# Kernel tuning notes

Measured on AMD Instinct MI355X. Metric: run time of the kernel, lower is better.

The kernel has to match this reference:

```python
import jax, jax.numpy as jnp
import numpy as np

B = 4096
INPUT_DIM = 4096
N_BLOCKS = 8
BLOCK = INPUT_DIM // N_BLOCKS  # 512
N_EXPERTS = 6
H = 1024   # expert_hidden
H2 = H // 2


def setup_inputs() -> dict:
    key = jax.random.key(0)
    ks = jax.random.split(key, 16)
    s = 0.02  # init scale keeps tanh/softmax in sane range
    return {
        "x":   jax.random.normal(ks[0], (B, INPUT_DIM), jnp.float32),
        # routers: per-block stacked weights [8, ...]
        "Wr1": jax.random.normal(ks[1], (N_BLOCKS, BLOCK, 32), jnp.float32) * s,
        "br1": jax.random.normal(ks[2], (N_BLOCKS, 32), jnp.float32) * s,
        "Wr2": jax.random.normal(ks[3], (N_BLOCKS, 32, N_EXPERTS), jnp.float32) * s,
        "br2": jax.random.normal(ks[4], (N_BLOCKS, N_EXPERTS), jnp.float32) * s,
        # experts: stacked [6, ...], shared across all 8 blocks
        "We1": jax.random.normal(ks[5], (N_EXPERTS, BLOCK, H), jnp.float32) * s,
        "be1": jax.random.normal(ks[6], (N_EXPERTS, H), jnp.float32) * s,
        "We2": jax.random.normal(ks[7], (N_EXPERTS, H, H2), jnp.float32) * s,
        "be2": jax.random.normal(ks[8], (N_EXPERTS, H2), jnp.float32) * s,
        "We3": jax.random.normal(ks[9], (N_EXPERTS, H2, 3), jnp.float32) * s,
        "be3": jax.random.normal(ks[10], (N_EXPERTS, 3), jnp.float32) * s,
        # aggregator
        "Wa1": jax.random.normal(ks[11], (3, 16), jnp.float32) * s,
        "ba1": jax.random.normal(ks[12], (16,), jnp.float32) * s,
        "Wa2": jax.random.normal(ks[13], (16, 3), jnp.float32) * s,
        "ba2": jax.random.normal(ks[14], (3,), jnp.float32) * s,
    }


def reference(x, Wr1, br1, Wr2, br2, We1, be1, We2, be2, We3, be3,
              Wa1, ba1, Wa2, ba2):
    b = x.shape[0]
    blocks = x.reshape(b, N_BLOCKS, BLOCK)                       # [b,s,d]
    # routers (one per block s)
    r1 = jax.nn.relu(jnp.einsum('bsd,sdh->bsh', blocks, Wr1) + br1)
    routing = jax.nn.softmax(
        jnp.einsum('bsh,she->bse', r1, Wr2) + br2, axis=-1)      # [b,s,E]
    # experts applied to every block (grouped GEMMs)
    h1 = jnp.tanh(jnp.einsum('bsd,edh->bseh', blocks, We1) + be1)        # [b,s,E,H]
    h2 = jnp.tanh(jnp.einsum('bseh,ehk->bsek', h1, We2) + be2)           # [b,s,E,H2]
    eo = jnp.einsum('bsek,eko->bseo', h2, We3) + be3                     # [b,s,E,3]
    weighted = jnp.einsum('bse,bseo->bso', routing, eo)                  # [b,s,3]
    final = weighted.mean(axis=1)                                        # mean over 8 blocks
    a1 = jax.nn.relu(final @ Wa1 + ba1)
    return a1 @ Wa2 + ba2                                                # [b,3]
```

## Files before the change

kernel.cpp:

```cpp
#include <hip/hip_runtime.h>
#include <cstdint>
#include <cstddef>

typedef __bf16 bf16;
typedef __bf16 bf16x4 __attribute__((ext_vector_type(4)));
typedef __bf16 bf16x8 __attribute__((ext_vector_type(8)));
typedef float  f32x4  __attribute__((ext_vector_type(4)));

#define NROWS   32768
#define DBLK    512
#define H1N     1024
#define H2N     512
#define NEXP    6
#define NBATCH  4096
#define HALL    (NEXP * H1N)

__device__ __forceinline__ void gld16(const void* g, void* l) {
    __builtin_amdgcn_global_load_lds(
        (const __attribute__((address_space(1))) void*)g,
        (__attribute__((address_space(3))) void*)l, 16, 0, 0);
}

__device__ __forceinline__ float fast_tanh(float x) {
    float e = __expf(2.0f * x);
    return 1.0f - __fdividef(2.0f, e + 1.0f);
}

__device__ __forceinline__ float hsum16(float v) {
    v += __shfl_xor(v, 1);
    v += __shfl_xor(v, 2);
    v += __shfl_xor(v, 4);
    v += __shfl_xor(v, 8);
    return v;
}

__device__ __forceinline__ int swz(int row, int g) {
    return row * 64 + ((g ^ (row & 7)) * 8);
}


__global__ void cvt_bf16_kernel(const float* __restrict__ in,
                                bf16* __restrict__ out, int n4) {
    int i = blockIdx.x * blockDim.x + threadIdx.x;
    if (i >= n4) return;
    float4 v = ((const float4*)in)[i];
    bf16x4 o;
    o.x = (bf16)v.x; o.y = (bf16)v.y; o.z = (bf16)v.z; o.w = (bf16)v.w;
    ((bf16x4*)out)[i] = o;
}

__global__ __launch_bounds__(256) void transpose_cvt(
    const float* __restrict__ in, bf16* __restrict__ out, int K, int N) {
    __shared__ bf16 tile[64][66];
    int e  = blockIdx.z;
    int n0 = blockIdx.x * 64;
    int k0 = blockIdx.y * 64;
    int c  = threadIdx.x & 63;
    int rb = threadIdx.x >> 6;
    const float* src = in + (size_t)e * K * N;
    bf16* dst = out + (size_t)e * N * K;
#pragma unroll
    for (int it = 0; it < 16; ++it) {
        int k = k0 + rb + it * 4;
        int n = n0 + c;
        if (k < K && n < N) tile[rb + it * 4][c] = (bf16)src[(size_t)k * N + n];
    }
    __syncthreads();
#pragma unroll
    for (int it = 0; it < 16; ++it) {
        int n = n0 + rb + it * 4;
        int k = k0 + c;
        if (n < N && k < K) dst[(size_t)n * K + k] = tile[c][rb + it * 4];
    }
}

__global__ void zero_f32_kernel(float* __restrict__ p, int n) {
    int i = blockIdx.x * blockDim.x + threadIdx.x;
    if (i < n) p[i] = 0.0f;
}


__global__ __launch_bounds__(256, 2) void router_kernel(
    const bf16* __restrict__ xbf,
    const bf16* __restrict__ Wr1t,
    const float* __restrict__ br1,
    const float* __restrict__ Wr2,
    const float* __restrict__ br2,
    float* __restrict__ routing) {
    __shared__ __align__(16) bf16 sA[128 * 64];
    __shared__ __align__(16) bf16 sB[32 * 64];
    const int tid = threadIdx.x;
    const int w = tid >> 6, l = tid & 63;
    const int s  = blockIdx.y;
    const int b0 = blockIdx.x * 128;
    const int wm = w * 32;
    const int srow = l >> 3, schk = (l & 7) * 8;
    const int fr = l & 15, fq = l >> 4;
    const bf16* Ab = xbf + (size_t)s * 512;
    const bf16* Bb = Wr1t + (size_t)s * (32 * 512);

    f32x4 acc[2][2];
#pragma unroll
    for (int i = 0; i < 2; ++i)
#pragma unroll
        for (int j = 0; j < 2; ++j) acc[i][j] = (f32x4){0.f, 0.f, 0.f, 0.f};

    for (int k0 = 0; k0 < 512; k0 += 64) {
        __syncthreads();
#pragma unroll
        for (int jj = 0; jj < 4; ++jj) {
            int row = w * 32 + jj * 8;
            gld16(Ab + (size_t)(b0 + row + srow) * 4096 + k0 + schk, sA + row * 64);
        }
        gld16(Bb + (size_t)(w * 8 + srow) * 512 + k0 + schk, sB + w * 8 * 64);
        __syncthreads();
#pragma unroll
        for (int ks = 0; ks < 2; ++ks) {
            bf16x8 af[2], bfr[2];
#pragma unroll
            for (int i = 0; i < 2; ++i)
                af[i] = *(const bf16x8*)&sA[(wm + i * 16 + fr) * 64 + ks * 32 + fq * 8];
#pragma unroll
            for (int j = 0; j < 2; ++j)
                bfr[j] = *(const bf16x8*)&sB[(j * 16 + fr) * 64 + ks * 32 + fq * 8];
#pragma unroll
            for (int i = 0; i < 2; ++i)
#pragma unroll
                for (int j = 0; j < 2; ++j)
                    acc[i][j] = __builtin_amdgcn_mfma_f32_16x16x32_bf16(
                        af[i], bfr[j], acc[i][j], 0, 0, 0);
        }
    }

    float b1v[2], w2v[2][6], br2v[6];
#pragma unroll
    for (int j = 0; j < 2; ++j) {
        int col = j * 16 + fr;
        b1v[j] = br1[s * 32 + col];
#pragma unroll
        for (int e2 = 0; e2 < 6; ++e2) w2v[j][e2] = Wr2[(s * 32 + col) * 6 + e2];
    }
#pragma unroll
    for (int e2 = 0; e2 < 6; ++e2) br2v[e2] = br2[s * 6 + e2];

#pragma unroll
    for (int i = 0; i < 2; ++i) {
#pragma unroll
        for (int r = 0; r < 4; ++r) {
            float lg[6] = {0.f, 0.f, 0.f, 0.f, 0.f, 0.f};
#pragma unroll
            for (int j = 0; j < 2; ++j) {
                float t = fmaxf(acc[i][j][r] + b1v[j], 0.f);
#pragma unroll
                for (int e2 = 0; e2 < 6; ++e2) lg[e2] += t * w2v[j][e2];
            }
#pragma unroll
            for (int e2 = 0; e2 < 6; ++e2) lg[e2] = hsum16(lg[e2]) + br2v[e2];
            float mx = lg[0];
#pragma unroll
            for (int e2 = 1; e2 < 6; ++e2) mx = fmaxf(mx, lg[e2]);
            float p[6], sum = 0.f;
#pragma unroll
            for (int e2 = 0; e2 < 6; ++e2) { p[e2] = __expf(lg[e2] - mx); sum += p[e2]; }
            float inv = __fdividef(1.f, sum);
            if (fr == 0) {
                int brow = b0 + wm + i * 16 + fq * 4 + r;
                float* dst = routing + ((size_t)brow * 8 + s) * 6;
#pragma unroll
                for (int e2 = 0; e2 < 6; ++e2) dst[e2] = p[e2] * inv;
            }
        }
    }
}

__global__ __launch_bounds__(256, 4) void gemm1_kernel(
    const bf16* __restrict__ A,
    const bf16* __restrict__ B,
    const float* __restrict__ bias,
    bf16* __restrict__ h1,
    int chunk_rows) {
    __shared__ __align__(16) bf16 sA[128 * 64];
    __shared__ __align__(16) bf16 sB[128 * 64];
    const int tid = threadIdx.x;
    const int w = tid >> 6, l = tid & 63;
    const int n0 = blockIdx.x * 128;
    const int m0 = blockIdx.y * 128;
    const int wm = (w & 1) * 64, wn = (w >> 1) * 64;
    const int srow = l >> 3;
    const int gcol = ((l & 7) ^ srow) * 8;
    const int fr = l & 15, fq = l >> 4;
    const int eb = m0 >> 10;
    bf16* h1e = h1 + (size_t)eb * chunk_rows * H1N;
    const int mloc = m0 & 1023;

    f32x4 acc[4][4];
#pragma unroll
    for (int i = 0; i < 4; ++i)
#pragma unroll
        for (int j = 0; j < 4; ++j) acc[i][j] = (f32x4){0.f, 0.f, 0.f, 0.f};

    for (int k0 = 0; k0 < DBLK; k0 += 64) {
        __syncthreads();
#pragma unroll
        for (int jj = 0; jj < 4; ++jj) {
            int row = w * 32 + jj * 8;
            gld16(A + (size_t)(m0 + row + srow) * DBLK + k0 + gcol, sA + row * 64);
            gld16(B + (size_t)(n0 + row + srow) * DBLK + k0 + gcol, sB + row * 64);
        }
        __syncthreads();
#pragma unroll
        for (int ks = 0; ks < 2; ++ks) {
            bf16x8 af[4], bfr[4];
#pragma unroll
            for (int i = 0; i < 4; ++i)
                af[i] = *(const bf16x8*)&sA[swz(wm + i * 16 + fr, ks * 4 + fq)];
#pragma unroll
            for (int j = 0; j < 4; ++j)
                bfr[j] = *(const bf16x8*)&sB[swz(wn + j * 16 + fr, ks * 4 + fq)];
#pragma unroll
            for (int i = 0; i < 4; ++i)
#pragma unroll
                for (int j = 0; j < 4; ++j)
                    acc[i][j] = __builtin_amdgcn_mfma_f32_16x16x32_bf16(
                        af[i], bfr[j], acc[i][j], 0, 0, 0);
        }
    }

#pragma unroll
    for (int i = 0; i < 4; ++i) {
        int colb = m0 + wm + i * 16 + fq * 4;
        int cloc = mloc + wm + i * 16 + fq * 4;
        float4 bb = *(const float4*)&bias[colb];
#pragma unroll
        for (int j = 0; j < 4; ++j) {
            int xrow = n0 + wn + j * 16 + fr;
            bf16x4 o;
            o.x = (bf16)fast_tanh(acc[i][j][0] + bb.x);
            o.y = (bf16)fast_tanh(acc[i][j][1] + bb.y);
            o.z = (bf16)fast_tanh(acc[i][j][2] + bb.z);
            o.w = (bf16)fast_tanh(acc[i][j][3] + bb.w);
            *(bf16x4*)&h1e[(size_t)xrow * H1N + cloc] = o;
        }
    }
}

__global__ __launch_bounds__(256, 4) void gemm2_kernel(
    const bf16* __restrict__ h1,
    const bf16* __restrict__ W2t,
    const float* __restrict__ be2,
    const float* __restrict__ We3,
    float* __restrict__ eo,
    int chunk_rows, int row0) {
    __shared__ __align__(16) bf16 sA[128 * 64];
    __shared__ __align__(16) bf16 sB[128 * 64];
    __shared__ float w3s[128 * 3];
    __shared__ float b2s[128];
    const int tid = threadIdx.x;
    const int w = tid >> 6, l = tid & 63;
    const int e  = blockIdx.z;
    const int n0 = blockIdx.x * 128;
    const int m0 = blockIdx.y * 128;
    const int wm = (w & 1) * 64, wn = (w >> 1) * 64;
    const int srow = l >> 3;
    const int gcol = ((l & 7) ^ srow) * 8;
    const int fr = l & 15, fq = l >> 4;
    const bf16* Ae = W2t + (size_t)e * (H2N * H1N);
    const bf16* Be = h1 + (size_t)e * chunk_rows * H1N;

    if (tid < 128) {
        int c = m0 + tid;
        b2s[tid] = be2[e * H2N + c];
        w3s[tid * 3 + 0] = We3[((size_t)e * H2N + c) * 3 + 0];
        w3s[tid * 3 + 1] = We3[((size_t)e * H2N + c) * 3 + 1];
        w3s[tid * 3 + 2] = We3[((size_t)e * H2N + c) * 3 + 2];
    }

    f32x4 acc[4][4];
#pragma unroll
    for (int i = 0; i < 4; ++i)
#pragma unroll
        for (int j = 0; j < 4; ++j) acc[i][j] = (f32x4){0.f, 0.f, 0.f, 0.f};

    for (int k0 = 0; k0 < H1N; k0 += 64) {
        __syncthreads();
#pragma unroll
        for (int jj = 0; jj < 4; ++jj) {
            int row = w * 32 + jj * 8;
            gld16(Ae + (size_t)(m0 + row + srow) * H1N + k0 + gcol, sA + row * 64);
            gld16(Be + (size_t)(n0 + row + srow) * H1N + k0 + gcol, sB + row * 64);
        }
        __syncthreads();
#pragma unroll
        for (int ks = 0; ks < 2; ++ks) {
            bf16x8 af[4], bfr[4];
#pragma unroll
            for (int i = 0; i < 4; ++i)
                af[i] = *(const bf16x8*)&sA[swz(wm + i * 16 + fr, ks * 4 + fq)];
#pragma unroll
            for (int j = 0; j < 4; ++j)
                bfr[j] = *(const bf16x8*)&sB[swz(wn + j * 16 + fr, ks * 4 + fq)];
#pragma unroll
            for (int i = 0; i < 4; ++i)
#pragma unroll
                for (int j = 0; j < 4; ++j)
                    acc[i][j] = __builtin_amdgcn_mfma_f32_16x16x32_bf16(
                        af[i], bfr[j], acc[i][j], 0, 0, 0);
        }
    }

    float p[4][3];
#pragma unroll
    for (int j = 0; j < 4; ++j) { p[j][0] = 0.f; p[j][1] = 0.f; p[j][2] = 0.f; }
#pragma unroll
    for (int i = 0; i < 4; ++i) {
        int cl = wm + i * 16 + fq * 4;
        float4 bb = *(const float4*)&b2s[cl];
        float4 wa = *(const float4*)&w3s[cl * 3 + 0];
        float4 wb = *(const float4*)&w3s[cl * 3 + 4];
        float4 wc = *(const float4*)&w3s[cl * 3 + 8];
        float bias4[4] = {bb.x, bb.y, bb.z, bb.w};
        float w30[4] = {wa.x, wa.w, wb.z, wc.y};
        float w31[4] = {wa.y, wb.x, wb.w, wc.z};
        float w32[4] = {wa.z, wb.y, wc.x, wc.w};
#pragma unroll
        for (int j = 0; j < 4; ++j) {
#pragma unroll
            for (int r = 0; r < 4; ++r) {
                float t = fast_tanh(acc[i][j][r] + bias4[r]);
                p[j][0] += t * w30[r];
                p[j][1] += t * w31[r];
                p[j][2] += t * w32[r];
            }
        }
    }
#pragma unroll
    for (int j = 0; j < 4; ++j) {
        float v0 = p[j][0], v1 = p[j][1], v2 = p[j][2];
        v0 += __shfl_xor(v0, 16); v0 += __shfl_xor(v0, 32);
        v1 += __shfl_xor(v1, 16); v1 += __shfl_xor(v1, 32);
        v2 += __shfl_xor(v2, 16); v2 += __shfl_xor(v2, 32);
        if (fq == 0) {
            int xrow = row0 + n0 + wn + j * 16 + fr;
            float* dst = eo + ((size_t)e * NROWS + xrow) * 3;
            atomicAdd(dst + 0, v0);
            atomicAdd(dst + 1, v1);
            atomicAdd(dst + 2, v2);
        }
    }
}

__global__ void final_kernel(
    const float* __restrict__ routing, const float* __restrict__ eo,
    const float* __restrict__ be3, const float* __restrict__ Wa1,
    const float* __restrict__ ba1, const float* __restrict__ Wa2,
    const float* __restrict__ ba2, float* __restrict__ out) {
    int b = blockIdx.x * blockDim.x + threadIdx.x;
    if (b >= NBATCH) return;
    float f0 = 0.f, f1 = 0.f, f2 = 0.f;
    for (int s = 0; s < 8; ++s) {
        int r = b * 8 + s;
        const float* rt = routing + (size_t)r * 6;
#pragma unroll
        for (int e = 0; e < 6; ++e) {
            float wgt = rt[e];
            const float* eop = eo + ((size_t)e * NROWS + r) * 3;
            f0 += wgt * (eop[0] + be3[e * 3 + 0]);
            f1 += wgt * (eop[1] + be3[e * 3 + 1]);
            f2 += wgt * (eop[2] + be3[e * 3 + 2]);
        }
    }
    f0 *= 0.125f; f1 *= 0.125f; f2 *= 0.125f;
    float o0 = ba2[0], o1 = ba2[1], o2 = ba2[2];
#pragma unroll
    for (int h = 0; h < 16; ++h) {
        float a = f0 * Wa1[h] + f1 * Wa1[16 + h] + f2 * Wa1[32 + h] + ba1[h];
        a = fmaxf(a, 0.f);
        o0 += a * Wa2[h * 3 + 0];
        o1 += a * Wa2[h * 3 + 1];
        o2 += a * Wa2[h * 3 + 2];
    }
    out[b * 3 + 0] = o0;
    out[b * 3 + 1] = o1;
    out[b * 3 + 2] = o2;
}


extern "C" void kernel_launch(void* const* d_in, const int* in_sizes, int n_in,
                              void* d_out, int out_size, void* d_ws, size_t ws_size,
                              hipStream_t stream) {
    const float* x   = (const float*)d_in[0];
    const float* Wr1 = (const float*)d_in[1];
    const float* br1 = (const float*)d_in[2];
    const float* Wr2 = (const float*)d_in[3];
    const float* br2 = (const float*)d_in[4];
    const float* We1 = (const float*)d_in[5];
    const float* be1 = (const float*)d_in[6];
    const float* We2 = (const float*)d_in[7];
    const float* be2 = (const float*)d_in[8];
    const float* We3 = (const float*)d_in[9];
    const float* be3 = (const float*)d_in[10];
    const float* Wa1 = (const float*)d_in[11];
    const float* ba1 = (const float*)d_in[12];
    const float* Wa2 = (const float*)d_in[13];
    const float* ba2 = (const float*)d_in[14];
    float* out = (float*)d_out;

    char* ws = (char*)d_ws;
    const size_t off_xbf  = 0;
    const size_t off_w1t  = off_xbf  + (size_t)33554432;
    const size_t off_w2t  = off_w1t  + (size_t)6291456;
    const size_t off_wr1t = off_w2t  + (size_t)6291456;
    const size_t off_rout = off_wr1t + (size_t)262144;
    const size_t off_eo   = off_rout + (size_t)786432;
    const size_t off_h1   = off_eo   + (size_t)2359296;

    int split = 1;
    while (split < 8 &&
           off_h1 + ((size_t)NROWS / split) * HALL * 2 > ws_size) split *= 2;
    if (off_h1 + ((size_t)NROWS / split) * HALL * 2 > ws_size) return;

    bf16*  xbf     = (bf16*)(ws + off_xbf);
    bf16*  W1t     = (bf16*)(ws + off_w1t);
    bf16*  W2t     = (bf16*)(ws + off_w2t);
    bf16*  Wr1t    = (bf16*)(ws + off_wr1t);
    float* routing = (float*)(ws + off_rout);
    float* eo      = (float*)(ws + off_eo);
    bf16*  h1      = (bf16*)(ws + off_h1);

    cvt_bf16_kernel<<<16384, 256, 0, stream>>>(x, xbf, 4194304);
    transpose_cvt<<<dim3(16, 8, 6), 256, 0, stream>>>(We1, W1t, 512, 1024);
    transpose_cvt<<<dim3(8, 16, 6), 256, 0, stream>>>(We2, W2t, 1024, 512);
    transpose_cvt<<<dim3(1, 8, 8), 256, 0, stream>>>(Wr1, Wr1t, 512, 32);
    zero_f32_kernel<<<2304, 256, 0, stream>>>(eo, 589824);

    router_kernel<<<dim3(32, 8), 256, 0, stream>>>(xbf, Wr1t, br1, Wr2, br2, routing);

    const int chunk_rows = NROWS / split;
    for (int c = 0; c < split; ++c) {
        const int row0 = c * chunk_rows;
        gemm1_kernel<<<dim3(chunk_rows / 128, HALL / 128), 256, 0, stream>>>(
            W1t, xbf + (size_t)row0 * DBLK, be1, h1, chunk_rows);
        gemm2_kernel<<<dim3(chunk_rows / 128, H2N / 128, NEXP), 256, 0, stream>>>(
            h1, W2t, be2, We3, eo, chunk_rows, row0);
    }

    final_kernel<<<16, 256, 0, stream>>>(routing, eo, be3, Wa1, ba1, Wa2, ba2, out);
}
```

Measured before the change: 762.9 us.

## Store h1 and We2 in FP8 and run second expert GEMM with FP8 MFMA

The first expert GEMM now writes the tanh activations h1 as packed FP8 instead of bf16, and We2 is transposed and quantized to FP8 with a fixed scale of 32. The second GEMM uses the FP8 MFMA instruction over byte tiles with a new LDS swizzle, and rescales the accumulator before bias and tanh. This halves h1 memory traffic and workspace (allowing fewer chunk splits) and uses the higher-throughput FP8 matrix path. The first GEMM's grid axes are swapped and occupancy hints are raised. The cost is reduced precision in both the activations and the weights.

```diff
diff --git a/kernel.cpp b/kernel.cpp
--- a/kernel.cpp
+++ b/kernel.cpp
@@ -6,6 +6,7 @@
 typedef __bf16 bf16x4 __attribute__((ext_vector_type(4)));
 typedef __bf16 bf16x8 __attribute__((ext_vector_type(8)));
 typedef float  f32x4  __attribute__((ext_vector_type(4)));
+typedef long long i64v;
 
 #define NROWS   32768
 #define DBLK    512
@@ -14,6 +15,8 @@
 #define NEXP    6
 #define NBATCH  4096
 #define HALL    (NEXP * H1N)
+#define W2SCALE 32.0f
+#define W2INV   0.03125f
 
 __device__ __forceinline__ void gld16(const void* g, void* l) {
     __builtin_amdgcn_global_load_lds(
@@ -36,6 +39,9 @@
 
 __device__ __forceinline__ int swz(int row, int g) {
     return row * 64 + ((g ^ (row & 7)) * 8);
+}
+__device__ __forceinline__ int swz8(int row, int g) {
+    return row * 64 + ((g ^ (row & 3)) << 4);
 }
 
 
@@ -71,6 +77,36 @@
         int n = n0 + rb + it * 4;
         int k = k0 + c;
         if (n < N && k < K) dst[(size_t)n * K + k] = tile[c][rb + it * 4];
+    }
+}
+
+__global__ __launch_bounds__(256) void transpose_cvt_fp8(
+    const float* __restrict__ in, uint8_t* __restrict__ out, int K, int N,
+    float scale) {
+    __shared__ float tile[64][65];
+    int e  = blockIdx.z;
+    int n0 = blockIdx.x * 64;
+    int k0 = blockIdx.y * 64;
+    int c  = threadIdx.x & 63;
+    int rb = threadIdx.x >> 6;
+    const float* src = in + (size_t)e * K * N;
+    uint8_t* dst = out + (size_t)e * N * K;
+#pragma unroll
+    for (int it = 0; it < 16; ++it) {
+        int k = k0 + rb + it * 4;
+        int n = n0 + c;
+        if (k < K && n < N) tile[rb + it * 4][c] = src[(size_t)k * N + n];
+    }
+    __syncthreads();
+#pragma unroll
+    for (int it = 0; it < 16; ++it) {
+        int n = n0 + rb + it * 4;
+        int k = k0 + c;
+        if (n < N && k < K) {
+            float v = tile[c][rb + it * 4] * scale;
+            int p = __builtin_amdgcn_cvt_pk_fp8_f32(v, v, 0, false);
+            dst[(size_t)n * K + k] = (uint8_t)(p & 0xff);
+        }
     }
 }
 
@@ -173,24 +209,24 @@
     }
 }
 
-__global__ __launch_bounds__(256, 4) void gemm1_kernel(
+__global__ __launch_bounds__(256, 5) void gemm1_kernel(
     const bf16* __restrict__ A,
     const bf16* __restrict__ B,
     const float* __restrict__ bias,
-    bf16* __restrict__ h1,
+    uint8_t* __restrict__ h1,
     int chunk_rows) {
     __shared__ __align__(16) bf16 sA[128 * 64];
     __shared__ __align__(16) bf16 sB[128 * 64];
     const int tid = threadIdx.x;
     const int w = tid >> 6, l = tid & 63;
-    const int n0 = blockIdx.x * 128;
-    const int m0 = blockIdx.y * 128;
+    const int m0 = blockIdx.x * 128;
+    const int n0 = blockIdx.y * 128;
     const int wm = (w & 1) * 64, wn = (w >> 1) * 64;
     const int srow = l >> 3;
     const int gcol = ((l & 7) ^ srow) * 8;
     const int fr = l & 15, fq = l >> 4;
     const int eb = m0 >> 10;
-    bf16* h1e = h1 + (size_t)eb * chunk_rows * H1N;
+    uint8_t* h1e = h1 + (size_t)eb * chunk_rows * H1N;
     const int mloc = m0 & 1023;
 
     f32x4 acc[4][4];
@@ -234,25 +270,27 @@
 #pragma unroll
         for (int j = 0; j < 4; ++j) {
             int xrow = n0 + wn + j * 16 + fr;
-            bf16x4 o;
-            o.x = (bf16)fast_tanh(acc[i][j][0] + bb.x);
-            o.y = (bf16)fast_tanh(acc[i][j][1] + bb.y);
-            o.z = (bf16)fast_tanh(acc[i][j][2] + bb.z);
-            o.w = (bf16)fast_tanh(acc[i][j][3] + bb.w);
-            *(bf16x4*)&h1e[(size_t)xrow * H1N + cloc] = o;
-        }
-    }
-}
-
-__global__ __launch_bounds__(256, 4) void gemm2_kernel(
-    const bf16* __restrict__ h1,
-    const bf16* __restrict__ W2t,
+            float t0 = fast_tanh(acc[i][j][0] + bb.x);
+            float t1 = fast_tanh(acc[i][j][1] + bb.y);
+            float t2 = fast_tanh(acc[i][j][2] + bb.z);
+            float t3 = fast_tanh(acc[i][j][3] + bb.w);
+            int p = 0;
+            p = __builtin_amdgcn_cvt_pk_fp8_f32(t0, t1, p, false);
+            p = __builtin_amdgcn_cvt_pk_fp8_f32(t2, t3, p, true);
+            *(uint32_t*)&h1e[(size_t)xrow * H1N + cloc] = (uint32_t)p;
+        }
+    }
+}
+
+__global__ __launch_bounds__(256, 5) void gemm2_kernel(
+    const uint8_t* __restrict__ h1,
+    const uint8_t* __restrict__ W2f8t,
     const float* __restrict__ be2,
     const float* __restrict__ We3,
     float* __restrict__ eo,
     int chunk_rows, int row0) {
-    __shared__ __align__(16) bf16 sA[128 * 64];
-    __shared__ __align__(16) bf16 sB[128 * 64];
+    __shared__ __align__(16) uint8_t sA[128 * 64];
+    __shared__ __align__(16) uint8_t sB[128 * 64];
     __shared__ float w3s[128 * 3];
     __shared__ float b2s[128];
     const int tid = threadIdx.x;
@@ -261,11 +299,11 @@
     const int n0 = blockIdx.x * 128;
     const int m0 = blockIdx.y * 128;
     const int wm = (w & 1) * 64, wn = (w >> 1) * 64;
-    const int srow = l >> 3;
-    const int gcol = ((l & 7) ^ srow) * 8;
+    const int srow4 = l >> 2;
+    const int g4 = (((l & 3) ^ (srow4 & 3)) << 4);
     const int fr = l & 15, fq = l >> 4;
-    const bf16* Ae = W2t + (size_t)e * (H2N * H1N);
-    const bf16* Be = h1 + (size_t)e * chunk_rows * H1N;
+    const uint8_t* Ae = W2f8t + (size_t)e * (H2N * H1N);
+    const uint8_t* Be = h1 + (size_t)e * chunk_rows * H1N;
 
     if (tid < 128) {
         int c = m0 + tid;
@@ -284,26 +322,30 @@
     for (int k0 = 0; k0 < H1N; k0 += 64) {
         __syncthreads();
 #pragma unroll
-        for (int jj = 0; jj < 4; ++jj) {
-            int row = w * 32 + jj * 8;
-            gld16(Ae + (size_t)(m0 + row + srow) * H1N + k0 + gcol, sA + row * 64);
-            gld16(Be + (size_t)(n0 + row + srow) * H1N + k0 + gcol, sB + row * 64);
+        for (int jj = 0; jj < 2; ++jj) {
+            int row = w * 32 + jj * 16 + srow4;
+            gld16(Ae + (size_t)(m0 + row) * H1N + k0 + g4, sA + (w * 32 + jj * 16) * 64);
+            gld16(Be + (size_t)(n0 + row) * H1N + k0 + g4, sB + (w * 32 + jj * 16) * 64);
         }
         __syncthreads();
 #pragma unroll
         for (int ks = 0; ks < 2; ++ks) {
-            bf16x8 af[4], bfr[4];
+            i64v af[4], bfr[4];
+#pragma unroll
+            for (int i = 0; i < 4; ++i) {
+                int row = wm + i * 16 + fr;
+                af[i] = *(const i64v*)&sA[swz8(row, ks * 2 + (fq >> 1)) + ((fq & 1) << 3)];
+            }
+#pragma unroll
+            for (int j = 0; j < 4; ++j) {
+                int row = wn + j * 16 + fr;
+                bfr[j] = *(const i64v*)&sB[swz8(row, ks * 2 + (fq >> 1)) + ((fq & 1) << 3)];
+            }
 #pragma unroll
             for (int i = 0; i < 4; ++i)
-                af[i] = *(const bf16x8*)&sA[swz(wm + i * 16 + fr, ks * 4 + fq)];
-#pragma unroll
-            for (int j = 0; j < 4; ++j)
-                bfr[j] = *(const bf16x8*)&sB[swz(wn + j * 16 + fr, ks * 4 + fq)];
-#pragma unroll
-            for (int i = 0; i < 4; ++i)
 #pragma unroll
                 for (int j = 0; j < 4; ++j)
-                    acc[i][j] = __builtin_amdgcn_mfma_f32_16x16x32_bf16(
+                    acc[i][j] = __builtin_amdgcn_mfma_f32_16x16x32_fp8_fp8(
                         af[i], bfr[j], acc[i][j], 0, 0, 0);
         }
     }
@@ -326,7 +368,7 @@
         for (int j = 0; j < 4; ++j) {
 #pragma unroll
             for (int r = 0; r < 4; ++r) {
-                float t = fast_tanh(acc[i][j][r] + bias4[r]);
+                float t = fast_tanh(acc[i][j][r] * W2INV + bias4[r]);
                 p[j][0] += t * w30[r];
                 p[j][1] += t * w31[r];
                 p[j][2] += t * w32[r];
@@ -416,20 +458,20 @@
 
     int split = 1;
     while (split < 8 &&
-           off_h1 + ((size_t)NROWS / split) * HALL * 2 > ws_size) split *= 2;
-    if (off_h1 + ((size_t)NROWS / split) * HALL * 2 > ws_size) return;
-
-    bf16*  xbf     = (bf16*)(ws + off_xbf);
-    bf16*  W1t     = (bf16*)(ws + off_w1t);
-    bf16*  W2t     = (bf16*)(ws + off_w2t);
-    bf16*  Wr1t    = (bf16*)(ws + off_wr1t);
-    float* routing = (float*)(ws + off_rout);
-    float* eo      = (float*)(ws + off_eo);
-    bf16*  h1      = (bf16*)(ws + off_h1);
+           off_h1 + ((size_t)NROWS / split) * HALL > ws_size) split *= 2;
+    if (off_h1 + ((size_t)NROWS / split) * HALL > ws_size) return;
+
+    bf16*    xbf     = (bf16*)(ws + off_xbf);
+    bf16*    W1t     = (bf16*)(ws + off_w1t);
+    uint8_t* W2f8t   = (uint8_t*)(ws + off_w2t);
+    bf16*    Wr1t    = (bf16*)(ws + off_wr1t);
+    float*   routing = (float*)(ws + off_rout);
+    float*   eo      = (float*)(ws + off_eo);
+    uint8_t* h1      = (uint8_t*)(ws + off_h1);
 
     cvt_bf16_kernel<<<16384, 256, 0, stream>>>(x, xbf, 4194304);
     transpose_cvt<<<dim3(16, 8, 6), 256, 0, stream>>>(We1, W1t, 512, 1024);
-    transpose_cvt<<<dim3(8, 16, 6), 256, 0, stream>>>(We2, W2t, 1024, 512);
+    transpose_cvt_fp8<<<dim3(8, 16, 6), 256, 0, stream>>>(We2, W2f8t, 1024, 512, W2SCALE);
     transpose_cvt<<<dim3(1, 8, 8), 256, 0, stream>>>(Wr1, Wr1t, 512, 32);
     zero_f32_kernel<<<2304, 256, 0, stream>>>(eo, 589824);
 
@@ -438,10 +480,10 @@
     const int chunk_rows = NROWS / split;
     for (int c = 0; c < split; ++c) {
         const int row0 = c * chunk_rows;
-        gemm1_kernel<<<dim3(chunk_rows / 128, HALL / 128), 256, 0, stream>>>(
+        gemm1_kernel<<<dim3(HALL / 128, chunk_rows / 128), 256, 0, stream>>>(
             W1t, xbf + (size_t)row0 * DBLK, be1, h1, chunk_rows);
         gemm2_kernel<<<dim3(chunk_rows / 128, H2N / 128, NEXP), 256, 0, stream>>>(
-            h1, W2t, be2, We3, eo, chunk_rows, row0);
+            h1, W2f8t, be2, We3, eo, chunk_rows, row0);
     }
 
     final_kernel<<<16, 256, 0, stream>>>(routing, eo, be3, Wa1, ba1, Wa2, ba2, out);
```

Result: slower. 1.121 ms (+47.0%).
